# Performance work log

Measured on AMD Instinct MI355X. Metric: run time of the kernel, lower is better.

## Reference

```python
import jax, jax.numpy as jnp
import numpy as np

IN_FEATURES = 4096
OUT_FEATURES = 11008
N_TOKENS = 8192


def setup_inputs() -> dict:
    key = jax.random.key(0)
    kx, kw, kb = jax.random.split(key, 3)
    x = jax.random.normal(kx, (N_TOKENS, IN_FEATURES), dtype=jnp.float32)
    # nn.Linear weight: [out_features, in_features]
    bound = 1.0 / np.sqrt(IN_FEATURES)
    weight = jax.random.uniform(kw, (OUT_FEATURES, IN_FEATURES), dtype=jnp.float32,
                                minval=-bound, maxval=bound)
    bias = jax.random.uniform(kb, (OUT_FEATURES,), dtype=jnp.float32,
                              minval=-bound, maxval=bound)
    return {"x": x, "weight": weight, "bias": bias}


def reference(x, weight, bias):
    # Ternarize weights to {-1, 0, +1} then standard dense matmul + bias.
    ternary_w = jnp.sign(weight)  # [out, in]
    return jnp.matmul(x, ternary_w.T) + bias  # [n_tokens, out]
```

## Files before the change

kernel.cpp:

```cpp
#include <hip/hip_runtime.h>
#include <stdint.h>

#define M_DIM 8192
#define N_DIM 11008
#define K_DIM 4096

#define BM 256
#define BN 256
#define BK 64
#define NT (K_DIM / BK)
#define GRID_M (M_DIM / BM)
#define GRID_N (N_DIM / BN)
#define NWG (GRID_M * GRID_N)

#define BUF (BM * BK)
#define NRING 5

typedef int i32x4 __attribute__((ext_vector_type(4)));

__device__ __forceinline__ void gload16(const int8_t* src, int8_t* dst) {
    __builtin_amdgcn_global_load_lds(
        (const __attribute__((address_space(1))) uint32_t*)src,
        (__attribute__((address_space(3))) uint32_t*)dst, 16, 0, 0);
}


__global__ __launch_bounds__(256) void quant_x_kernel(
    const float* __restrict__ x, int8_t* __restrict__ xq, float* __restrict__ sinv)
{
    const int wave = blockIdx.x * 4 + (threadIdx.x >> 6);
    const int lane = threadIdx.x & 63;
    const float* row = x + (size_t)wave * K_DIM;

    float4 v[16];
    float mx = 0.0f;
    #pragma unroll
    for (int j = 0; j < 16; ++j) {
        v[j] = *(const float4*)(row + (j * 64 + lane) * 4);
        mx = fmaxf(mx, fmaxf(fmaxf(fabsf(v[j].x), fabsf(v[j].y)),
                             fmaxf(fabsf(v[j].z), fabsf(v[j].w))));
    }
    #pragma unroll
    for (int off = 32; off > 0; off >>= 1)
        mx = fmaxf(mx, __shfl_xor(mx, off));
    if (mx < 1e-30f) mx = 1e-30f;
    const float s = 127.0f / mx;

    int8_t* orow = xq + (size_t)wave * K_DIM;
    #pragma unroll
    for (int j = 0; j < 16; ++j) {
        int a = (int)__builtin_rintf(v[j].x * s);
        int b = (int)__builtin_rintf(v[j].y * s);
        int c = (int)__builtin_rintf(v[j].z * s);
        int d = (int)__builtin_rintf(v[j].w * s);
        uint32_t p = (uint32_t)(a & 0xFF) | ((uint32_t)(b & 0xFF) << 8) |
                     ((uint32_t)(c & 0xFF) << 16) | ((uint32_t)(d & 0xFF) << 24);
        *(uint32_t*)(orow + (j * 64 + lane) * 4) = p;
    }
    if (lane == 0) sinv[wave] = mx / 127.0f;
}


__global__ __launch_bounds__(256) void sign_w_kernel(
    const float* __restrict__ w, int8_t* __restrict__ wq, long long n16)
{
    long long i = (long long)blockIdx.x * blockDim.x + threadIdx.x;
    const long long stride = (long long)gridDim.x * blockDim.x;
    for (; i < n16; i += stride) {
        const float* src = w + i * 16;
        uint32_t pk[4];
        #pragma unroll
        for (int q = 0; q < 4; ++q) {
            float4 f = *(const float4*)(src + q * 4);
            int a = (f.x > 0.f) ? 1 : ((f.x < 0.f) ? -1 : 0);
            int b = (f.y > 0.f) ? 1 : ((f.y < 0.f) ? -1 : 0);
            int c = (f.z > 0.f) ? 1 : ((f.z < 0.f) ? -1 : 0);
            int d = (f.w > 0.f) ? 1 : ((f.w < 0.f) ? -1 : 0);
            pk[q] = (uint32_t)(a & 0xFF) | ((uint32_t)(b & 0xFF) << 8) |
                    ((uint32_t)(c & 0xFF) << 16) | ((uint32_t)(d & 0xFF) << 24);
        }
        *(i32x4*)(wq + i * 16) = (i32x4){(int)pk[0], (int)pk[1], (int)pk[2], (int)pk[3]};
    }
}


__global__ __launch_bounds__(512, 2) void ternary_gemm_i8(
    const int8_t* __restrict__ A, const int8_t* __restrict__ B,
    const float* __restrict__ bias, const float* __restrict__ sinv,
    float* __restrict__ out)
{
    extern __shared__ int8_t lds[];
    int8_t* As = lds;
    int8_t* Bs = lds + NRING * BUF;

    const int tid  = threadIdx.x;
    const int lane = tid & 63;
    const int wid  = tid >> 6;
    const int wm   = wid >> 2;
    const int wn   = wid & 3;
    const int l15  = lane & 15;
    const int l4   = lane >> 4;

    const int bid = blockIdx.x;
    const int swz = (bid & 7) * (NWG / 8) + (bid >> 3);
    const int bm  = swz / GRID_N;
    const int bn  = swz % GRID_N;
    const long brow = (long)bm * BM;
    const long bcol = (long)bn * BN;

    const int rowt = tid >> 2;
    const int ssrc = (tid & 3) ^ ((tid >> 3) & 3);
    const int8_t* pA = A + (size_t)(brow + rowt) * K_DIM + ssrc * 16;
    const int8_t* pB = B + (size_t)(bcol + rowt) * K_DIM + ssrc * 16;

    auto stageA2 = [&](int t, int bslot) {
        #pragma unroll
        for (int r = 0; r < 2; ++r)
            gload16(pA + (size_t)r * 128 * K_DIM + (size_t)t * BK,
                    As + bslot * BUF + r * 8192 + wid * 1024 + (lane << 4));
    };
    auto stageB2 = [&](int t, int bslot) {
        #pragma unroll
        for (int r = 0; r < 2; ++r)
            gload16(pB + (size_t)r * 128 * K_DIM + (size_t)t * BK,
                    Bs + bslot * BUF + r * 8192 + wid * 1024 + (lane << 4));
    };

    const int slot = l4 ^ ((l15 >> 1) & 3);
    const int aOff = (wm * 16 + l15) * 64 + slot * 16;
    const int bOff = (wn * 16 + l15) * 64 + slot * 16;

    i32x4 acc[8][4];
    #pragma unroll
    for (int m = 0; m < 8; ++m)
        #pragma unroll
        for (int n = 0; n < 4; ++n) acc[m][n] = (i32x4){0, 0, 0, 0};

    i32x4 arA[8], brA[4], arB[8], brB[4];

    stageA2(0, 0); stageB2(0, 0);
    stageA2(1, 1); stageB2(1, 1);
    stageA2(2, 2); stageB2(2, 2);
    stageA2(3, 3); stageB2(3, 3);
    asm volatile("s_waitcnt vmcnt(8)" ::: "memory");
    __builtin_amdgcn_s_barrier();
    __builtin_amdgcn_sched_barrier(0);
    {
        const int8_t* Ab = As;
        const int8_t* Bb = Bs;
        #pragma unroll
        for (int n = 0; n < 4; ++n) brA[n] = *(const i32x4*)(Bb + n * 4096 + bOff);
        #pragma unroll
        for (int m = 0; m < 8; ++m) arA[m] = *(const i32x4*)(Ab + m * 2048 + aOff);
    }
    __builtin_amdgcn_sched_barrier(0);

    int sn = 1;
    int ss = 4;

    auto body = [&](int t, i32x4 (&arc)[8], i32x4 (&brc)[4],
                           i32x4 (&arn)[8], i32x4 (&brn)[4]) {
        const int8_t* An = As + sn * BUF;
        const int8_t* Bn = Bs + sn * BUF;
        const bool rd = (t + 1 < NT);
        const bool st = (t + 4 < NT);

        __builtin_amdgcn_s_setprio(1);
        #pragma unroll
        for (int m = 0; m < 2; ++m)
            #pragma unroll
            for (int n = 0; n < 4; ++n)
                acc[m][n] = __builtin_amdgcn_mfma_i32_16x16x64_i8(arc[m], brc[n], acc[m][n], 0, 0, 0);
        __builtin_amdgcn_s_setprio(0);
        if (rd) {
            brn[0] = *(const i32x4*)(Bn + 0 * 4096 + bOff);
            brn[1] = *(const i32x4*)(Bn + 1 * 4096 + bOff);
            brn[2] = *(const i32x4*)(Bn + 2 * 4096 + bOff);
            brn[3] = *(const i32x4*)(Bn + 3 * 4096 + bOff);
            arn[0] = *(const i32x4*)(An + 0 * 2048 + aOff);
        }
        __builtin_amdgcn_sched_barrier(0);

        __builtin_amdgcn_s_setprio(1);
        #pragma unroll
        for (int m = 2; m < 4; ++m)
            #pragma unroll
            for (int n = 0; n < 4; ++n)
                acc[m][n] = __builtin_amdgcn_mfma_i32_16x16x64_i8(arc[m], brc[n], acc[m][n], 0, 0, 0);
        __builtin_amdgcn_s_setprio(0);
        if (rd) {
            arn[1] = *(const i32x4*)(An + 1 * 2048 + aOff);
            arn[2] = *(const i32x4*)(An + 2 * 2048 + aOff);
            arn[3] = *(const i32x4*)(An + 3 * 2048 + aOff);
        }
        __builtin_amdgcn_sched_barrier(0);

        __builtin_amdgcn_s_setprio(1);
        #pragma unroll
        for (int m = 4; m < 6; ++m)
            #pragma unroll
            for (int n = 0; n < 4; ++n)
                acc[m][n] = __builtin_amdgcn_mfma_i32_16x16x64_i8(arc[m], brc[n], acc[m][n], 0, 0, 0);
        __builtin_amdgcn_s_setprio(0);
        if (rd) {
            arn[4] = *(const i32x4*)(An + 4 * 2048 + aOff);
            arn[5] = *(const i32x4*)(An + 5 * 2048 + aOff);
        }
        if (st) stageA2(t + 4, ss);
        __builtin_amdgcn_sched_barrier(0);

        __builtin_amdgcn_s_setprio(1);
        #pragma unroll
        for (int m = 6; m < 8; ++m)
            #pragma unroll
            for (int n = 0; n < 4; ++n)
                acc[m][n] = __builtin_amdgcn_mfma_i32_16x16x64_i8(arc[m], brc[n], acc[m][n], 0, 0, 0);
        __builtin_amdgcn_s_setprio(0);
        if (rd) {
            arn[6] = *(const i32x4*)(An + 6 * 2048 + aOff);
            arn[7] = *(const i32x4*)(An + 7 * 2048 + aOff);
        }
        if (st) stageB2(t + 4, ss);
        __builtin_amdgcn_sched_barrier(0);

        if (t <= NT - 5)      { asm volatile("s_waitcnt vmcnt(8)" ::: "memory"); }
        else if (t == NT - 4) { asm volatile("s_waitcnt vmcnt(4)" ::: "memory"); }
        else                  { asm volatile("s_waitcnt vmcnt(0)" ::: "memory"); }
        __builtin_amdgcn_s_barrier();
        __builtin_amdgcn_sched_barrier(0);

        sn = (sn == NRING - 1) ? 0 : sn + 1;
        ss = (ss == NRING - 1) ? 0 : ss + 1;
    };

    for (int t = 0; t < NT; t += 2) {
        body(t,     arA, brA, arB, brB);
        body(t + 1, arB, brB, arA, brA);
    }

    int   cols[4];
    float bv[4];
    #pragma unroll
    for (int n = 0; n < 4; ++n) {
        cols[n] = (int)bcol + n * 64 + wn * 16 + l15;
        bv[n] = bias[cols[n]];
    }
    #pragma unroll
    for (int m = 0; m < 8; ++m) {
        const size_t row0 = (size_t)brow + m * 32 + wm * 16 + l4 * 4;
        float s0 = sinv[row0], s1 = sinv[row0 + 1], s2 = sinv[row0 + 2], s3 = sinv[row0 + 3];
        #pragma unroll
        for (int n = 0; n < 4; ++n) {
            out[(row0 + 0) * N_DIM + cols[n]] = (float)acc[m][n][0] * s0 + bv[n];
            out[(row0 + 1) * N_DIM + cols[n]] = (float)acc[m][n][1] * s1 + bv[n];
            out[(row0 + 2) * N_DIM + cols[n]] = (float)acc[m][n][2] * s2 + bv[n];
            out[(row0 + 3) * N_DIM + cols[n]] = (float)acc[m][n][3] * s3 + bv[n];
        }
    }
}


__global__ void naive_kernel(const float* __restrict__ x, const float* __restrict__ w,
                             const float* __restrict__ bias, float* __restrict__ out) {
    long long o = (long long)blockIdx.x * blockDim.x + threadIdx.x;
    if (o >= (long long)M_DIM * N_DIM) return;
    int row = (int)(o / N_DIM), col = (int)(o % N_DIM);
    float s = 0.0f;
    const float* xr = x + (size_t)row * K_DIM;
    const float* wr = w + (size_t)col * K_DIM;
    for (int k = 0; k < K_DIM; ++k) {
        float wv = wr[k];
        s += (wv > 0.0f) ? xr[k] : ((wv < 0.0f) ? -xr[k] : 0.0f);
    }
    out[o] = s + bias[col];
}


extern "C" void kernel_launch(void* const* d_in, const int* in_sizes, int n_in,
                              void* d_out, int out_size, void* d_ws, size_t ws_size,
                              hipStream_t stream) {
    const float* x    = (const float*)d_in[0];
    const float* w    = (const float*)d_in[1];
    const float* bias = (const float*)d_in[2];
    float* out        = (float*)d_out;

    const size_t xq_bytes = (size_t)M_DIM * K_DIM;
    const size_t wq_bytes = (size_t)N_DIM * K_DIM;
    const size_t si_bytes = (size_t)M_DIM * sizeof(float);

    if (ws_size >= xq_bytes + wq_bytes + si_bytes) {
        int8_t* xq   = (int8_t*)d_ws;
        int8_t* wq   = (int8_t*)((char*)d_ws + xq_bytes);
        float*  sinv = (float*)((char*)d_ws + xq_bytes + wq_bytes);

        quant_x_kernel<<<M_DIM / 4, 256, 0, stream>>>(x, xq, sinv);
        const long long n16 = ((long long)N_DIM * K_DIM) / 16;
        sign_w_kernel<<<2048, 256, 0, stream>>>(w, wq, n16);

        const int lds_bytes = NRING * 2 * BUF;
        hipFuncSetAttribute(reinterpret_cast<const void*>(ternary_gemm_i8),
                            hipFuncAttributeMaxDynamicSharedMemorySize, lds_bytes);
        ternary_gemm_i8<<<NWG, 512, lds_bytes, stream>>>(xq, wq, bias, sinv, out);
    } else {
        const long long total = (long long)M_DIM * N_DIM;
        naive_kernel<<<(int)((total + 255) / 256), 256, 0, stream>>>(x, w, bias, out);
    }
}
```

Before: 470.2 us.

## Load B operand directly from global into registers, bypassing LDS staging

Removes the LDS ring for the weight (B) operand. Each wave now fetches its B fragments with direct global_load_dwordx4 into registers one k-step ahead, and the wait counts are reworked to match. This halves LDS usage and removes the LDS write and read traffic for B. In exchange, B data shared between the two wm waves is fetched twice from the cache hierarchy. Global latency must also now hide behind a single k-step of MFMAs, and the new vmcnt waits effectively shorten the A prefetch depth.

```diff
diff --git a/kernel.cpp b/kernel.cpp
--- a/kernel.cpp
+++ b/kernel.cpp
@@ -22,6 +22,13 @@
     __builtin_amdgcn_global_load_lds(
         (const __attribute__((address_space(1))) uint32_t*)src,
         (__attribute__((address_space(3))) uint32_t*)dst, 16, 0, 0);
+}
+
+__device__ __forceinline__ i32x4 bload(const int8_t* base, uint32_t voff) {
+    i32x4 r;
+    asm volatile("global_load_dwordx4 %0, %1, %2"
+                 : "=v"(r) : "v"(voff), "s"(base) : "memory");
+    return r;
 }
 
 
@@ -91,7 +98,6 @@
 {
     extern __shared__ int8_t lds[];
     int8_t* As = lds;
-    int8_t* Bs = lds + NRING * BUF;
 
     const int tid  = threadIdx.x;
     const int lane = tid & 63;
@@ -111,7 +117,6 @@
     const int rowt = tid >> 2;
     const int ssrc = (tid & 3) ^ ((tid >> 3) & 3);
     const int8_t* pA = A + (size_t)(brow + rowt) * K_DIM + ssrc * 16;
-    const int8_t* pB = B + (size_t)(bcol + rowt) * K_DIM + ssrc * 16;
 
     auto stageA2 = [&](int t, int bslot) {
         #pragma unroll
@@ -119,16 +124,15 @@
             gload16(pA + (size_t)r * 128 * K_DIM + (size_t)t * BK,
                     As + bslot * BUF + r * 8192 + wid * 1024 + (lane << 4));
     };
-    auto stageB2 = [&](int t, int bslot) {
-        #pragma unroll
-        for (int r = 0; r < 2; ++r)
-            gload16(pB + (size_t)r * 128 * K_DIM + (size_t)t * BK,
-                    Bs + bslot * BUF + r * 8192 + wid * 1024 + (lane << 4));
-    };
 
     const int slot = l4 ^ ((l15 >> 1) & 3);
     const int aOff = (wm * 16 + l15) * 64 + slot * 16;
-    const int bOff = (wn * 16 + l15) * 64 + slot * 16;
+
+    uint32_t vb[4];
+    #pragma unroll
+    for (int n = 0; n < 4; ++n)
+        vb[n] = (uint32_t)(((uint32_t)(bcol + n * 64 + wn * 16 + l15)) * (uint32_t)K_DIM
+                           + (uint32_t)(l4 * 16));
 
     i32x4 acc[8][4];
     #pragma unroll
@@ -138,21 +142,14 @@
 
     i32x4 arA[8], brA[4], arB[8], brB[4];
 
-    stageA2(0, 0); stageB2(0, 0);
-    stageA2(1, 1); stageB2(1, 1);
-    stageA2(2, 2); stageB2(2, 2);
-    stageA2(3, 3); stageB2(3, 3);
-    asm volatile("s_waitcnt vmcnt(8)" ::: "memory");
+    #pragma unroll
+    for (int n = 0; n < 4; ++n) { brA[n] = bload(B, vb[n]); vb[n] += 64; }
+    stageA2(0, 0); stageA2(1, 1); stageA2(2, 2); stageA2(3, 3);
+    asm volatile("s_waitcnt vmcnt(4)" ::: "memory");
     __builtin_amdgcn_s_barrier();
     __builtin_amdgcn_sched_barrier(0);
-    {
-        const int8_t* Ab = As;
-        const int8_t* Bb = Bs;
-        #pragma unroll
-        for (int n = 0; n < 4; ++n) brA[n] = *(const i32x4*)(Bb + n * 4096 + bOff);
-        #pragma unroll
-        for (int m = 0; m < 8; ++m) arA[m] = *(const i32x4*)(Ab + m * 2048 + aOff);
-    }
+    #pragma unroll
+    for (int m = 0; m < 8; ++m) arA[m] = *(const i32x4*)(As + m * 2048 + aOff);
     __builtin_amdgcn_sched_barrier(0);
 
     int sn = 1;
@@ -161,10 +158,12 @@
     auto body = [&](int t, i32x4 (&arc)[8], i32x4 (&brc)[4],
                            i32x4 (&arn)[8], i32x4 (&brn)[4]) {
         const int8_t* An = As + sn * BUF;
-        const int8_t* Bn = Bs + sn * BUF;
         const bool rd = (t + 1 < NT);
         const bool st = (t + 4 < NT);
 
+        if (t <= NT - 4) { asm volatile("s_waitcnt vmcnt(2)" ::: "memory"); }
+        else             { asm volatile("s_waitcnt vmcnt(0)" ::: "memory"); }
+        __builtin_amdgcn_sched_barrier(0);
         __builtin_amdgcn_s_setprio(1);
         #pragma unroll
         for (int m = 0; m < 2; ++m)
@@ -173,11 +172,10 @@
                 acc[m][n] = __builtin_amdgcn_mfma_i32_16x16x64_i8(arc[m], brc[n], acc[m][n], 0, 0, 0);
         __builtin_amdgcn_s_setprio(0);
         if (rd) {
-            brn[0] = *(const i32x4*)(Bn + 0 * 4096 + bOff);
-            brn[1] = *(const i32x4*)(Bn + 1 * 4096 + bOff);
-            brn[2] = *(const i32x4*)(Bn + 2 * 4096 + bOff);
-            brn[3] = *(const i32x4*)(Bn + 3 * 4096 + bOff);
+            #pragma unroll
+            for (int n = 0; n < 4; ++n) { brn[n] = bload(B, vb[n]); vb[n] += 64; }
             arn[0] = *(const i32x4*)(An + 0 * 2048 + aOff);
+            arn[1] = *(const i32x4*)(An + 1 * 2048 + aOff);
         }
         __builtin_amdgcn_sched_barrier(0);
 
@@ -189,7 +187,6 @@
                 acc[m][n] = __builtin_amdgcn_mfma_i32_16x16x64_i8(arc[m], brc[n], acc[m][n], 0, 0, 0);
         __builtin_amdgcn_s_setprio(0);
         if (rd) {
-            arn[1] = *(const i32x4*)(An + 1 * 2048 + aOff);
             arn[2] = *(const i32x4*)(An + 2 * 2048 + aOff);
             arn[3] = *(const i32x4*)(An + 3 * 2048 + aOff);
         }
@@ -220,12 +217,8 @@
             arn[6] = *(const i32x4*)(An + 6 * 2048 + aOff);
             arn[7] = *(const i32x4*)(An + 7 * 2048 + aOff);
         }
-        if (st) stageB2(t + 4, ss);
-        __builtin_amdgcn_sched_barrier(0);
-
-        if (t <= NT - 5)      { asm volatile("s_waitcnt vmcnt(8)" ::: "memory"); }
-        else if (t == NT - 4) { asm volatile("s_waitcnt vmcnt(4)" ::: "memory"); }
-        else                  { asm volatile("s_waitcnt vmcnt(0)" ::: "memory"); }
+        __builtin_amdgcn_sched_barrier(0);
+
         __builtin_amdgcn_s_barrier();
         __builtin_amdgcn_sched_barrier(0);
 
@@ -297,7 +290,7 @@
         const long long n16 = ((long long)N_DIM * K_DIM) / 16;
         sign_w_kernel<<<2048, 256, 0, stream>>>(w, wq, n16);
 
-        const int lds_bytes = NRING * 2 * BUF;
+        const int lds_bytes = NRING * BUF;
         hipFuncSetAttribute(reinterpret_cast<const void*>(ternary_gemm_i8),
                             hipFuncAttributeMaxDynamicSharedMemorySize, lds_bytes);
         ternary_gemm_i8<<<NWG, 512, lds_bytes, stream>>>(xq, wq, bias, sinv, out);
```

New measurement: 570.2 us. 21.3% more time.
